# Optimization experiments

Measured on AMD Instinct MI355X. Metric: run time of the kernel, lower is better.

Reference implementation:

```python
import jax, jax.numpy as jnp
import numpy as np

D = 1024          # input_dim
H = 16            # num_heads
S = 2             # scalar
MAX_LEN = 2048
HEAD_DIM = D // H // S      # 32
DV = D // H                 # 64, value head dim
SCALING = (D // H) ** -0.5


def setup_inputs() -> dict:
    key = jax.random.key(0)
    k1, k2, k3, k4, k5, k6 = jax.random.split(key, 6)
    L, B = 2046, 4
    input_tensor = jax.random.normal(k1, (L, B, D), dtype=jnp.float32)
    # k_v_proj: Linear(MAX_LEN, MAX_LEN // S); bias exists but is unused in forward
    w_kv = jax.random.normal(k2, (MAX_LEN // S, MAX_LEN), dtype=jnp.float32) / np.sqrt(MAX_LEN)
    # q_proj: Linear(D, D // S)
    w_q = jax.random.normal(k3, (D // S, D), dtype=jnp.float32) / np.sqrt(D)
    b_q = jax.random.normal(k4, (D // S,), dtype=jnp.float32) * 0.01
    # out_proj: Linear(D, D)
    w_out = jax.random.normal(k5, (D, D), dtype=jnp.float32) / np.sqrt(D)
    b_out = jax.random.normal(k6, (D,), dtype=jnp.float32) * 0.01
    return {"input_tensor": input_tensor, "w_kv": w_kv, "w_q": w_q,
            "b_q": b_q, "w_out": w_out, "b_out": b_out}


def reference(input_tensor, w_kv, w_q, b_q, w_out, b_out):
    L, B, _ = input_tensor.shape
    P = L // S + 1                       # projected (low-rank) sequence length
    X = jnp.transpose(input_tensor, (1, 0, 2))        # [B, L, D]
    q = X @ w_q.T + b_q                                # [B, L, D/S]
    Wp = w_kv.T[:L, :P]                                # [L, P] sequence projection
    v = jnp.einsum('bld,lp->bdp', X, Wp)               # [B, D, P]
    k = jnp.einsum('blc,lp->bcp', q, Wp)               # [B, D/S, P]
    q = q * SCALING
    # q: b l (h d) -> b h l d
    qh = q.reshape(B, L, H, HEAD_DIM).transpose(0, 2, 1, 3)
    # k: b (d h) p -> b h d p   (d outer, h inner in the channel split)
    kh = k.reshape(B, HEAD_DIM, H, P).transpose(0, 2, 1, 3)
    # v: b (d h) p -> b h p d
    vh = v.reshape(B, DV, H, P).transpose(0, 2, 3, 1)
    attn = jnp.einsum('bhld,bhdp->bhlp', qh, kh)       # [B, H, L, P]
    attn = jax.nn.softmax(attn.astype(jnp.float32), axis=-1).astype(attn.dtype)
    out = jnp.einsum('bhlp,bhpd->bhld', attn, vh)      # [B, H, L, DV]
    # (b h) l d -> b l (d h): d outer, h inner in concat
    out = out.transpose(0, 2, 3, 1).reshape(B, L, D)
    out = out @ w_out.T + b_out                        # [B, L, D]
    return jnp.transpose(out, (1, 0, 2))               # [L, B, D]
```

## Files before the change

### kernel.cpp

```cpp
#include <hip/hip_runtime.h>
#include <hip/hip_bf16.h>

typedef long long i64;
typedef unsigned int uint;
using u16 = unsigned short;
using f32x4  = __attribute__((ext_vector_type(4))) float;
using bf16x8 = __attribute__((ext_vector_type(8))) short;
using u32x4  = __attribute__((ext_vector_type(4))) uint;
using u16x4  = __attribute__((ext_vector_type(4))) u16;

#define QSCALE 0.18033688011112042f

#if __has_builtin(__builtin_amdgcn_exp2f)
#define EXP2(x) __builtin_amdgcn_exp2f(x)
#else
#define EXP2(x) __builtin_exp2f(x)
#endif

__device__ __forceinline__ u16 f2b(float x) {
    uint u = __float_as_uint(x);
    return (u16)((u + 0x7FFFu + ((u >> 16) & 1u)) >> 16);
}
__device__ __forceinline__ float b2f(u16 h) {
    return __uint_as_float((uint)h << 16);
}
__device__ __forceinline__ uint cvt_pk_bf16(float lo, float hi) {
    uint r;
    asm("v_cvt_pk_bf16_f32 %0, %1, %2" : "=v"(r) : "v"(lo), "v"(hi));
    return r;
}

__global__ __launch_bounds__(256) void conv_pad(
    const float* __restrict__ src, u16* __restrict__ dst,
    int M_valid, int K_valid, int kshift, int s_row)
{
    i64 i = (i64)blockIdx.x * 256 + threadIdx.x;
    int m = (int)(i >> (kshift - 2));
    int k = ((int)(i & ((1 << (kshift - 2)) - 1))) << 2;
    u16x4 hv;
    #pragma unroll
    for (int j = 0; j < 4; ++j) {
        int kk = k + j;
        float x = (m < M_valid && kk < K_valid) ? src[(i64)m * s_row + kk] : 0.f;
        hv[j] = f2b(x);
    }
    *(u16x4*)(dst + ((i64)m << kshift) + k) = hv;
}

__global__ __launch_bounds__(256) void conv_wout_perm(
    const float* __restrict__ w, u16* __restrict__ dst)
{
    int i = blockIdx.x * 256 + threadIdx.x;
    int n = i >> 8, kp4 = (i & 255) << 2;
    u16x4 hv;
    #pragma unroll
    for (int j = 0; j < 4; ++j) {
        int kp = kp4 + j;
        hv[j] = f2b(w[((i64)n << 10) + ((kp & 63) << 4) + (kp >> 6)]);
    }
    *(u16x4*)(dst + ((i64)n << 10) + kp4) = hv;
}

__global__ __launch_bounds__(256) void build_kvA(
    const u16* __restrict__ Xb, const u16* __restrict__ qu,
    u16* __restrict__ dst)
{
    const int b = blockIdx.z, r0 = blockIdx.y * 64, l0 = blockIdx.x * 64;
    const int tid = threadIdx.x;
    __shared__ float ts[64][65];
    #pragma unroll
    for (int t = 0; t < 16; ++t) {
        int idx = t * 256 + tid;
        int ch = idx & 63, lr = idx >> 6;
        int lg = l0 + lr;
        float v = 0.f;
        if (lg < 2046) {
            if (r0 < 1024) v = b2f(Xb[((i64)lg * 4 + b) * 1024 + (r0 + ch)]);
            else           v = b2f(qu[((i64)lg * 4 + b) * 512 + (r0 - 1024 + ch)]);
        }
        ts[lr][ch] = v;
    }
    __syncthreads();
    #pragma unroll
    for (int t = 0; t < 16; ++t) {
        int idx = t * 256 + tid;
        int ll = idx & 63, rl = idx >> 6;
        dst[((i64)b * 1536 + r0 + rl) * 2048 + l0 + ll] = f2b(ts[ll][rl]);
    }
}

template<int MODE>
__global__ __launch_bounds__(256) void gemm_bf16(
    const u16* __restrict__ A, i64 a_bs,
    const u16* __restrict__ Bm,
    float* __restrict__ C, const float* __restrict__ bias,
    u16* __restrict__ x0, u16* __restrict__ x1,
    int Krow, int KT, int M_valid)
{
    __shared__ __align__(16) u16 As[8192], Bs[8192];
    const int tid = threadIdx.x, lane = tid & 63, w = tid >> 6;
    const int fr = lane & 15, g = lane >> 4;

    const int fid = blockIdx.x;
    const int xcd = fid & 7, s = fid >> 3;
    int nb, mb, bz;
    if (MODE == 0)      { nb = s & 3; mb = xcd * 8 + (s >> 2); bz = 0; }
    else if (MODE == 1) { nb = s & 7; int pr = xcd * 6 + (s >> 3); bz = pr / 12; mb = pr % 12; }
    else                { nb = s & 7; int pr = xcd * 8 + (s >> 3); bz = pr >> 4; mb = pr & 15; }

    const u16* src = (w < 2)
        ? (A + (i64)bz * a_bs + ((i64)mb * 128 + (w & 1) * 64) * Krow)
        : (Bm + ((i64)nb * 128 + (w & 1) * 64) * Krow);
    u16* dstb = (w < 2) ? As : Bs;
    const int R0 = (w & 1) * 64;
    const int lr8 = lane >> 3, lc8 = lane & 7;
    const u16* src_lane = src + (i64)lr8 * Krow + ((lc8 ^ lr8) << 3);
    char* wbase = (char*)dstb + (R0 + lr8) * 128 + lc8 * 16;

    f32x4 acc[4][4];
    #pragma unroll
    for (int i = 0; i < 4; ++i)
        #pragma unroll
        for (int j = 0; j < 4; ++j)
            acc[i][j] = (f32x4){0.f, 0.f, 0.f, 0.f};

    u32x4 st[8];
    #pragma unroll
    for (int it = 0; it < 8; ++it)
        st[it] = *(const u32x4*)(src_lane + (i64)(it * 8) * Krow);

    const int wr = (w >> 1) * 64, wc = (w & 1) * 64;

    for (int kt = 0; kt < KT; ++kt) {
        __syncthreads();
        #pragma unroll
        for (int it = 0; it < 8; ++it)
            *(u32x4*)(wbase + it * 1024) = st[it];
        __syncthreads();
        if (kt + 1 < KT) {
            #pragma unroll
            for (int it = 0; it < 8; ++it)
                st[it] = *(const u32x4*)(src_lane + (i64)(it * 8) * Krow
                                                  + (kt + 1) * 64);
        }
        #pragma unroll
        for (int half = 0; half < 2; ++half) {
            bf16x8 ah[4], bh[4];
            const int co = ((half * 4 + g) ^ (fr & 7)) << 4;
            #pragma unroll
            for (int mi = 0; mi < 4; ++mi) {
                int rr = wr + mi * 16 + fr;
                ah[mi] = *(const bf16x8*)((const char*)As + rr * 128 + co);
            }
            #pragma unroll
            for (int ni = 0; ni < 4; ++ni) {
                int rr = wc + ni * 16 + fr;
                bh[ni] = *(const bf16x8*)((const char*)Bs + rr * 128 + co);
            }
            #pragma unroll
            for (int mi = 0; mi < 4; ++mi)
                #pragma unroll
                for (int ni = 0; ni < 4; ++ni)
                    acc[mi][ni] = __builtin_amdgcn_mfma_f32_16x16x32_bf16(
                        ah[mi], bh[ni], acc[mi][ni], 0, 0, 0);
        }
    }

    #pragma unroll
    for (int mi = 0; mi < 4; ++mi)
        #pragma unroll
        for (int ni = 0; ni < 4; ++ni) {
            int gm0 = mb * 128 + wr + mi * 16 + g * 4;
            int gn  = nb * 128 + wc + ni * 16 + fr;
            #pragma unroll
            for (int r = 0; r < 4; ++r) {
                int gm = gm0 + r;
                float val = acc[mi][ni][r];
                if (MODE == 0) {
                    x0[(i64)gm * 512 + gn] = f2b(val + bias[gn]);
                } else if (MODE == 1) {
                    if (gm < 1024) {
                        int e = gm >> 4, hh = gm & 15;
                        i64 so = ((i64)(bz * 16 + hh) * 64 + e) * 1024
                               + (gn & ~31) + (((gn >> 2) & 3) << 3)
                               + (gn & 3) + (((gn >> 4) & 1) << 2);
                        x1[so] = f2b(val);
                    } else {
                        int c2 = gm - 1024, d = c2 >> 4, hh = c2 & 15;
                        x0[((i64)(bz * 16 + hh) * 1024 + gn) * 32 + d] = f2b(val);
                    }
                } else {
                    if (gm < M_valid)
                        C[(i64)bz * 1024 + (i64)gm * 4096 + gn] = val + bias[gn];
                }
            }
        }
}

__global__ __launch_bounds__(256) void attn_mfma(
    const u16* __restrict__ qu, const u16* __restrict__ kT,
    const u16* __restrict__ vT, u16* __restrict__ attA)
{
    const int g0 = blockIdx.x;
    const int xcd = g0 & 7, sub = g0 >> 3;
    const int lblk = sub & 15;
    const int bh = xcd + ((sub >> 4) << 3);
    const int b = bh >> 4, h = bh & 15;
    const int tid = threadIdx.x, lane = tid & 63, w = tid >> 6;
    const int fr = lane & 15, g = lane >> 4;
    const int l0 = lblk * 128 + w * 32;

    __shared__ __align__(16) u16 kbuf[2][2560];
    __shared__ __align__(16) u16 vbuf[2][4608];

    bf16x8 aq[2];
    #pragma unroll
    for (int mf = 0; mf < 2; ++mf)
        aq[mf] = *(const bf16x8*)(qu + ((i64)((l0 + mf * 16 + fr) * 4 + b) * 512
                                        + h * 32 + g * 8));

    const f32x4 zf = {0.f, 0.f, 0.f, 0.f};

    const int sr = tid >> 2, sc = tid & 3;
    const u16* ksrc = kT + (i64)bh * 32768 + sr * 32 + sc * 8;
    char* kdst = (char*)&kbuf[0][0] + sr * 80 + sc * 16;
    const u16* vsrc = vT + (i64)bh * 65536 + (i64)sr * 1024 + sc * 8;
    char* vdst = (char*)&vbuf[0][0] + sr * 144 + sc * 16;

    *(u32x4*)kdst = *(const u32x4*)ksrc;
    *(u32x4*)vdst = *(const u32x4*)vsrc;
    *(u32x4*)(vdst + 64) = *(const u32x4*)(vsrc + 32);
    __syncthreads();

    float l_part[2] = {0.f, 0.f};
    f32x4 o[2][4];
    #pragma unroll
    for (int mf = 0; mf < 2; ++mf)
        #pragma unroll
        for (int nf = 0; nf < 4; ++nf)
            o[mf][nf] = zf;

    for (int t = 0; t < 16; ++t) {
        const int cur = t & 1;
        const int tn = (t < 15) ? t + 1 : 15;

        u32x4 knx  = *(const u32x4*)(ksrc + tn * 2048);
        u32x4 vnx0 = *(const u32x4*)(vsrc + tn * 64);
        u32x4 vnx1 = *(const u32x4*)(vsrc + tn * 64 + 32);

        const char* kc_ = (const char*)&kbuf[cur][0];
        f32x4 s[2][4];
        __builtin_amdgcn_s_setprio(1);
        #pragma unroll
        for (int nf = 0; nf < 4; ++nf) {
            bf16x8 ak = *(const bf16x8*)(kc_ + (nf * 16 + fr) * 80 + g * 16);
            s[0][nf] = __builtin_amdgcn_mfma_f32_16x16x32_bf16(ak, aq[0], zf, 0, 0, 0);
            s[1][nf] = __builtin_amdgcn_mfma_f32_16x16x32_bf16(ak, aq[1], zf, 0, 0, 0);
        }
        __builtin_amdgcn_s_setprio(0);

        u32x4 ppk[2][2];
        #pragma unroll
        for (int mf = 0; mf < 2; ++mf)
            #pragma unroll
            for (int nf = 0; nf < 4; ++nf) {
                float p_[4];
                #pragma unroll
                for (int r = 0; r < 4; ++r) p_[r] = EXP2(QSCALE * s[mf][nf][r]);
                l_part[mf] += (p_[0] + p_[1]) + (p_[2] + p_[3]);
                ppk[mf][nf >> 1][(nf & 1) * 2 + 0] = cvt_pk_bf16(p_[0], p_[1]);
                ppk[mf][nf >> 1][(nf & 1) * 2 + 1] = cvt_pk_bf16(p_[2], p_[3]);
            }

        {
            const int nb_ = cur ^ 1;
            *(u32x4*)(kdst + nb_ * 5120) = knx;
            *(u32x4*)(vdst + nb_ * 9216) = vnx0;
            *(u32x4*)(vdst + nb_ * 9216 + 64) = vnx1;
        }

        const char* vc_ = (const char*)&vbuf[cur][0];
        __builtin_amdgcn_s_setprio(1);
        #pragma unroll
        for (int ks = 0; ks < 2; ++ks) {
            bf16x8 ap0 = __builtin_bit_cast(bf16x8, ppk[0][ks]);
            bf16x8 ap1 = __builtin_bit_cast(bf16x8, ppk[1][ks]);
            #pragma unroll
            for (int nf = 0; nf < 4; ++nf) {
                bf16x8 bv = *(const bf16x8*)(vc_ + (nf * 16 + fr) * 144
                                                 + ks * 64 + g * 16);
                o[0][nf] = __builtin_amdgcn_mfma_f32_16x16x32_bf16(ap0, bv, o[0][nf], 0, 0, 0);
                o[1][nf] = __builtin_amdgcn_mfma_f32_16x16x32_bf16(ap1, bv, o[1][nf], 0, 0, 0);
            }
        }
        __builtin_amdgcn_s_setprio(0);

        __syncthreads();
    }

    #pragma unroll
    for (int mf = 0; mf < 2; ++mf) {
        l_part[mf] += __shfl_xor(l_part[mf], 16);
        l_part[mf] += __shfl_xor(l_part[mf], 32);
    }
    #pragma unroll
    for (int mf = 0; mf < 2; ++mf)
        #pragma unroll
        for (int r = 0; r < 4; ++r) {
            int l = l0 + mf * 16 + g * 4 + r;
            float tot = __shfl(l_part[mf], g * 4 + r);
            if (l < 2046) {
                float inv = 1.f / tot;
                #pragma unroll
                for (int nf = 0; nf < 4; ++nf)
                    attA[((i64)b * 2048 + l) * 1024 + h * 64 + nf * 16 + fr]
                        = f2b(o[mf][nf][r] * inv);
            }
        }
}

extern "C" void kernel_launch(void* const* d_in, const int* in_sizes, int n_in,
                              void* d_out, int out_size, void* d_ws, size_t ws_size,
                              hipStream_t stream) {
    const float* input = (const float*)d_in[0];
    const float* w_kv  = (const float*)d_in[1];
    const float* w_q   = (const float*)d_in[2];
    const float* b_q   = (const float*)d_in[3];
    const float* w_out = (const float*)d_in[4];
    const float* b_out = (const float*)d_in[5];
    float* out = (float*)d_out;

    char* W = (char*)d_ws;
    u16* Xb      = (u16*)(W + 16777216);
    u16* qu      = (u16*)(W + 33554432);
    u16* wq_b    = (u16*)(W + 41943040);
    u16* wkv_b   = (u16*)(W + 42991616);
    u16* wout_b  = (u16*)(W + 47185920);
    u16* kvA     = (u16*)(W + 49283072);
    u16* kT      = (u16*)(W + 74448896);
    u16* vT      = (u16*)(W + 78643200);
    u16* attA    = (u16*)(W + 87031808);

    dim3 blk(256);

    conv_pad<<<8192, blk, 0, stream>>>(input, Xb, 8184, 1024, 10, 1024);
    conv_pad<<<512,  blk, 0, stream>>>(w_q, wq_b, 512, 1024, 10, 1024);
    conv_pad<<<2048, blk, 0, stream>>>(w_kv, wkv_b, 1024, 2046, 11, 2048);
    conv_wout_perm<<<1024, blk, 0, stream>>>(w_out, wout_b);

    gemm_bf16<0><<<dim3(256), blk, 0, stream>>>(
        Xb, 0, wq_b, nullptr, b_q, qu, nullptr, 1024, 16, 8192);

    build_kvA<<<dim3(32, 24, 4), blk, 0, stream>>>(Xb, qu, kvA);

    gemm_bf16<1><<<dim3(384), blk, 0, stream>>>(
        kvA, (i64)1536 * 2048, wkv_b, nullptr, nullptr, kT, vT, 2048, 32, 1536);

    attn_mfma<<<dim3(1024), blk, 0, stream>>>(qu, kT, vT, attA);

    gemm_bf16<2><<<dim3(512), blk, 0, stream>>>(
        attA, (i64)2048 * 1024, wout_b, out, b_out, nullptr, nullptr, 1024, 16, 2046);
}
```

Before: 184.7 us.

## Load GEMM MFMA fragments directly from global memory, dropping LDS staging

```diff
diff --git a/kernel.cpp b/kernel.cpp
--- a/kernel.cpp
+++ b/kernel.cpp
@@ -97,25 +97,36 @@
     u16* __restrict__ x0, u16* __restrict__ x1,
     int Krow, int KT, int M_valid)
 {
-    __shared__ __align__(16) u16 As[8192], Bs[8192];
     const int tid = threadIdx.x, lane = tid & 63, w = tid >> 6;
     const int fr = lane & 15, g = lane >> 4;
 
     const int fid = blockIdx.x;
     const int xcd = fid & 7, s = fid >> 3;
     int nb, mb, bz;
-    if (MODE == 0)      { nb = s & 3; mb = xcd * 8 + (s >> 2); bz = 0; }
-    else if (MODE == 1) { nb = s & 7; int pr = xcd * 6 + (s >> 3); bz = pr / 12; mb = pr % 12; }
-    else                { nb = s & 7; int pr = xcd * 8 + (s >> 3); bz = pr >> 4; mb = pr & 15; }
-
-    const u16* src = (w < 2)
-        ? (A + (i64)bz * a_bs + ((i64)mb * 128 + (w & 1) * 64) * Krow)
-        : (Bm + ((i64)nb * 128 + (w & 1) * 64) * Krow);
-    u16* dstb = (w < 2) ? As : Bs;
-    const int R0 = (w & 1) * 64;
-    const int lr8 = lane >> 3, lc8 = lane & 7;
-    const u16* src_lane = src + (i64)lr8 * Krow + ((lc8 ^ lr8) << 3);
-    char* wbase = (char*)dstb + (R0 + lr8) * 128 + lc8 * 16;
+    if (MODE == 0)      { nb = s & 1; mb = xcd * 16 + (s >> 1); bz = 0; }
+    else if (MODE == 1) { nb = (xcd & 1) * 2 + (s & 1);
+                          int pr = (xcd >> 1) * 24 + (s >> 1); bz = pr / 24; mb = pr % 24; }
+    else                { nb = s & 3; int pr = xcd * 16 + (s >> 2); bz = pr >> 5; mb = pr & 31; }
+
+    const u16* Ab = A + (i64)bz * a_bs + ((i64)(mb * 64) + fr) * Krow + g * 8;
+    const u16* Bb = Bm + ((i64)(nb * 256 + w * 64) + fr) * Krow + g * 8;
+
+#define LOADF(d, t) do { \
+        _Pragma("unroll") \
+        for (int mi = 0; mi < 4; ++mi) \
+            d[mi] = *(const bf16x8*)(Ab + (i64)(mi * 16) * Krow + (t) * 32); \
+        _Pragma("unroll") \
+        for (int ni = 0; ni < 4; ++ni) \
+            d[4 + ni] = *(const bf16x8*)(Bb + (i64)(ni * 16) * Krow + (t) * 32); \
+    } while (0)
+#define MF(f) do { \
+        _Pragma("unroll") \
+        for (int mi = 0; mi < 4; ++mi) \
+            _Pragma("unroll") \
+            for (int ni = 0; ni < 4; ++ni) \
+                acc[mi][ni] = __builtin_amdgcn_mfma_f32_16x16x32_bf16( \
+                    f[mi], f[4 + ni], acc[mi][ni], 0, 0, 0); \
+    } while (0)
 
     f32x4 acc[4][4];
     #pragma unroll
@@ -124,54 +135,23 @@
         for (int j = 0; j < 4; ++j)
             acc[i][j] = (f32x4){0.f, 0.f, 0.f, 0.f};
 
-    u32x4 st[8];
-    #pragma unroll
-    for (int it = 0; it < 8; ++it)
-        st[it] = *(const u32x4*)(src_lane + (i64)(it * 8) * Krow);
-
-    const int wr = (w >> 1) * 64, wc = (w & 1) * 64;
-
-    for (int kt = 0; kt < KT; ++kt) {
-        __syncthreads();
-        #pragma unroll
-        for (int it = 0; it < 8; ++it)
-            *(u32x4*)(wbase + it * 1024) = st[it];
-        __syncthreads();
-        if (kt + 1 < KT) {
-            #pragma unroll
-            for (int it = 0; it < 8; ++it)
-                st[it] = *(const u32x4*)(src_lane + (i64)(it * 8) * Krow
-                                                  + (kt + 1) * 64);
-        }
-        #pragma unroll
-        for (int half = 0; half < 2; ++half) {
-            bf16x8 ah[4], bh[4];
-            const int co = ((half * 4 + g) ^ (fr & 7)) << 4;
-            #pragma unroll
-            for (int mi = 0; mi < 4; ++mi) {
-                int rr = wr + mi * 16 + fr;
-                ah[mi] = *(const bf16x8*)((const char*)As + rr * 128 + co);
-            }
-            #pragma unroll
-            for (int ni = 0; ni < 4; ++ni) {
-                int rr = wc + ni * 16 + fr;
-                bh[ni] = *(const bf16x8*)((const char*)Bs + rr * 128 + co);
-            }
-            #pragma unroll
-            for (int mi = 0; mi < 4; ++mi)
-                #pragma unroll
-                for (int ni = 0; ni < 4; ++ni)
-                    acc[mi][ni] = __builtin_amdgcn_mfma_f32_16x16x32_bf16(
-                        ah[mi], bh[ni], acc[mi][ni], 0, 0, 0);
-        }
-    }
+    bf16x8 fe[8], fo[8];
+    LOADF(fe, 0);
+    for (int kt = 0; kt < KT; kt += 2) {
+        LOADF(fo, kt + 1);
+        MF(fe);
+        if (kt + 2 < KT) LOADF(fe, kt + 2);
+        MF(fo);
+    }
+#undef LOADF
+#undef MF
 
     #pragma unroll
     for (int mi = 0; mi < 4; ++mi)
         #pragma unroll
         for (int ni = 0; ni < 4; ++ni) {
-            int gm0 = mb * 128 + wr + mi * 16 + g * 4;
-            int gn  = nb * 128 + wc + ni * 16 + fr;
+            int gm0 = mb * 64 + mi * 16 + g * 4;
+            int gn  = nb * 256 + w * 64 + ni * 16 + fr;
             #pragma unroll
             for (int r = 0; r < 4; ++r) {
                 int gm = gm0 + r;
@@ -349,15 +329,15 @@
     conv_wout_perm<<<1024, blk, 0, stream>>>(w_out, wout_b);
 
     gemm_bf16<0><<<dim3(256), blk, 0, stream>>>(
-        Xb, 0, wq_b, nullptr, b_q, qu, nullptr, 1024, 16, 8192);
+        Xb, 0, wq_b, nullptr, b_q, qu, nullptr, 1024, 32, 8192);
 
     build_kvA<<<dim3(32, 24, 4), blk, 0, stream>>>(Xb, qu, kvA);
 
     gemm_bf16<1><<<dim3(384), blk, 0, stream>>>(
-        kvA, (i64)1536 * 2048, wkv_b, nullptr, nullptr, kT, vT, 2048, 32, 1536);
+        kvA, (i64)1536 * 2048, wkv_b, nullptr, nullptr, kT, vT, 2048, 64, 1536);
 
     attn_mfma<<<dim3(1024), blk, 0, stream>>>(qu, kT, vT, attA);
 
     gemm_bf16<2><<<dim3(512), blk, 0, stream>>>(
-        attA, (i64)2048 * 1024, wout_b, out, b_out, nullptr, nullptr, 1024, 16, 2046);
-}
+        attA, (i64)2048 * 1024, wout_b, out, b_out, nullptr, nullptr, 1024, 32, 2046);
+}
```

After: 317.2 us. +71.7%, slower.
